# Kernel optimization log

Hardware: AMD Instinct MI355X
Metric: run time of the kernel (lower is better)

## Reference

```python
import jax, jax.numpy as jnp
import numpy as np

HIDDEN = 4096
NUM_Q = 32
NUM_KV = 8
HEAD_DIM = 128
EPS = 1e-6
ROPE_THETA = 1e6


def _rmsnorm(x, w):
    # x: [..., HEAD_DIM]
    var = jnp.mean(x * x, axis=-1, keepdims=True)
    return x * jax.lax.rsqrt(var + EPS) * w


def _rope(x, positions):
    # x: [n_tok, H, HEAD_DIM], rotate-half convention
    half = HEAD_DIM // 2
    inv_freq = 1.0 / (ROPE_THETA ** (jnp.arange(0, half, dtype=jnp.float32) / half))
    freqs = positions.astype(jnp.float32)[:, None] * inv_freq  # [n_tok, half]
    cos = jnp.concatenate([jnp.cos(freqs), jnp.cos(freqs)], axis=-1)[:, None, :]
    sin = jnp.concatenate([jnp.sin(freqs), jnp.sin(freqs)], axis=-1)[:, None, :]
    x1, x2 = x[..., :half], x[..., half:]
    rot = jnp.concatenate([-x2, x1], axis=-1)
    return x * cos + rot * sin


def setup_inputs() -> dict:
    key = jax.random.key(0)
    ks = jax.random.split(key, 7)
    n_tok = 2048
    s = 0.02
    return {
        "hidden": jax.random.normal(ks[0], (n_tok, HIDDEN), dtype=jnp.float32),
        "positions": jnp.arange(n_tok, dtype=jnp.int32),
        "Wq": jax.random.normal(ks[1], (HIDDEN, NUM_Q * HEAD_DIM), dtype=jnp.float32) * s,
        "Wk": jax.random.normal(ks[2], (HIDDEN, NUM_KV * HEAD_DIM), dtype=jnp.float32) * s,
        "Wv": jax.random.normal(ks[3], (HIDDEN, NUM_KV * HEAD_DIM), dtype=jnp.float32) * s,
        "Wo": jax.random.normal(ks[4], (NUM_Q * HEAD_DIM, HIDDEN), dtype=jnp.float32) * s,
        "q_norm_w": jnp.ones((HEAD_DIM,), dtype=jnp.float32),
        "k_norm_w": jnp.ones((HEAD_DIM,), dtype=jnp.float32),
    }


def reference(hidden, positions, Wq, Wk, Wv, Wo, q_norm_w, k_norm_w):
    n_tok = hidden.shape[0]
    group = NUM_Q // NUM_KV

    q = (hidden @ Wq).reshape(n_tok, NUM_Q, HEAD_DIM)
    k = (hidden @ Wk).reshape(n_tok, NUM_KV, HEAD_DIM)
    v = (hidden @ Wv).reshape(n_tok, NUM_KV, HEAD_DIM)

    q = _rmsnorm(q, q_norm_w)
    k = _rmsnorm(k, k_norm_w)
    q = _rope(q, positions)
    k = _rope(k, positions)

    # GQA: group q heads [n_tok, NUM_KV, group, HEAD_DIM]
    qg = q.reshape(n_tok, NUM_KV, group, HEAD_DIM)
    scale = 1.0 / np.sqrt(HEAD_DIM)
    scores = jnp.einsum("qhgd,khd->hgqk", qg, k) * scale  # [NUM_KV, group, n_tok, n_tok]
    causal = jnp.tril(jnp.ones((n_tok, n_tok), dtype=bool))
    scores = jnp.where(causal, scores, jnp.finfo(scores.dtype).min)
    probs = jax.nn.softmax(scores, axis=-1)
    out = jnp.einsum("hgqk,khd->qhgd", probs, v)  # [n_tok, NUM_KV, group, HEAD_DIM]
    out = out.reshape(n_tok, NUM_Q * HEAD_DIM)
    return out @ Wo
```

## Files before the change

kernel.cpp:

```cpp
#include <hip/hip_runtime.h>
#include <stdint.h>

typedef unsigned short u16;
typedef __bf16 bf16_t;
typedef bf16_t bf16x8 __attribute__((ext_vector_type(8)));
typedef float f32x4 __attribute__((ext_vector_type(4)));
typedef u16 u16x4 __attribute__((ext_vector_type(4)));
typedef u16 u16x8 __attribute__((ext_vector_type(8)));

#define HIDDEN 4096
#define NTOK 2048
#define NQ 32
#define NKV 8
#define HD 128
#define QKV_N 6144

#define AS1 __attribute__((address_space(1)))
#define AS3 __attribute__((address_space(3)))

__device__ __forceinline__ u16 f2bf(float f) {
  union { float f; uint32_t u; } v; v.f = f;
  uint32_t u = v.u;
  return (u16)((u + 0x7fffu + ((u >> 16) & 1u)) >> 16);
}

__global__ void cvt_hidden(const float* __restrict__ src, u16* __restrict__ dst, int n4) {
  int i = blockIdx.x * blockDim.x + threadIdx.x;
  if (i >= n4) return;
  float4 v = ((const float4*)src)[i];
  u16x4 o;
  o[0] = f2bf(v.x); o[1] = f2bf(v.y); o[2] = f2bf(v.z); o[3] = f2bf(v.w);
  ((u16x4*)dst)[i] = o;
}

__global__ void transpose_cvt(const float* __restrict__ src, u16* __restrict__ dst,
                              int R, int C) {
  __shared__ float tile[64][65];
  int tx = threadIdx.x & 63;
  int ty = threadIdx.x >> 6;
  int r0 = blockIdx.y * 64, c0 = blockIdx.x * 64;
  for (int i = 0; i < 16; i++) {
    int r = ty + i * 4;
    tile[r][tx] = src[(size_t)(r0 + r) * C + c0 + tx];
  }
  __syncthreads();
  for (int i = 0; i < 16; i++) {
    int c = ty + i * 4;
    dst[(size_t)(c0 + c) * R + r0 + tx] = f2bf(tile[tx][c]);
  }
}

__global__ __launch_bounds__(256, 3) void gemm_bt(const u16* __restrict__ A,
                                                  const u16* __restrict__ B,
                                                  float* __restrict__ C,
                                                  int M, int N, int K) {
  __shared__ u16 sA[128 * 64];
  __shared__ u16 sB[128 * 64];
  const int tid = threadIdx.x;
  const int wave = tid >> 6, lane = tid & 63;
  const int quad = lane >> 4, l16 = lane & 15;
  const int wy = wave >> 1, wx = wave & 1;
  const int row0 = blockIdx.y * 128, col0 = blockIdx.x * 128;
  f32x4 acc[4][4] = {};
  const int lr = lane >> 3;
  const int sc = (lane & 7) ^ lr;
  const u16* gA = A + (size_t)(row0 + wave * 32 + lr) * K + sc * 8;
  const u16* gB = B + (size_t)(col0 + wave * 32 + lr) * K + sc * 8;
  u16* lA = sA + wave * 32 * 64;
  u16* lB = sB + wave * 32 * 64;
  const int swz = l16 & 7;
  for (int k0 = 0; k0 < K; k0 += 64) {
    for (int j = 0; j < 4; j++) {
      __builtin_amdgcn_global_load_lds(
          (AS1 void*)(void*)(gA + k0 + (size_t)(j * 8) * K),
          (AS3 void*)(void*)(lA + j * 8 * 64), 16, 0, 0);
      __builtin_amdgcn_global_load_lds(
          (AS1 void*)(void*)(gB + k0 + (size_t)(j * 8) * K),
          (AS3 void*)(void*)(lB + j * 8 * 64), 16, 0, 0);
    }
    __syncthreads();
    bf16x8 af[2][4], bfr[2][4];
    for (int s = 0; s < 2; s++)
      for (int mi = 0; mi < 4; mi++) {
        const int c = ((s * 4 + quad) ^ swz) * 8;
        af[s][mi] = *(const bf16x8*)(const void*)(sA + (wy * 64 + mi * 16 + l16) * 64 + c);
        bfr[s][mi] = *(const bf16x8*)(const void*)(sB + (wx * 64 + mi * 16 + l16) * 64 + c);
      }
    for (int s = 0; s < 2; s++)
      for (int mi = 0; mi < 4; mi++)
        for (int ni = 0; ni < 4; ni++)
          acc[mi][ni] = __builtin_amdgcn_mfma_f32_16x16x32_bf16(af[s][mi], bfr[s][ni], acc[mi][ni], 0, 0, 0);
    __syncthreads();
  }
  for (int mi = 0; mi < 4; mi++)
    for (int ni = 0; ni < 4; ni++) {
      int row = row0 + wy * 64 + mi * 16 + quad * 4;
      int col = col0 + wx * 64 + ni * 16 + l16;
      float* cp = C + (size_t)row * N + col;
      for (int r = 0; r < 4; r++) cp[(size_t)r * N] = acc[mi][ni][r];
    }
}

__global__ void normrope(const float* __restrict__ qkv, const int* __restrict__ pos,
                         const float* __restrict__ qw, const float* __restrict__ kw,
                         u16* __restrict__ Qo, u16* __restrict__ Ko) {
  const int hh = blockIdx.x;
  const int t = blockIdx.y * 4 + (threadIdx.x >> 6);
  const int lane = threadIdx.x & 63;
  const bool isQ = hh < NQ;
  const int col = isQ ? hh * HD : HIDDEN + (hh - NQ) * HD;
  const float* src = qkv + (size_t)t * QKV_N + col;
  float x1 = src[lane], x2 = src[lane + 64];
  float ss = x1 * x1 + x2 * x2;
  for (int m = 1; m < 64; m <<= 1) ss += __shfl_xor(ss, m);
  float inv = rsqrtf(ss * (1.0f / 128.0f) + 1e-6f);
  const float* w = isQ ? qw : kw;
  x1 *= inv * w[lane];
  x2 *= inv * w[lane + 64];
  float p = (float)pos[t];
  float freq = expf((float)lane * -0.2158673525f);
  float a = p * freq;
  float sn = sinf(a), cs = cosf(a);
  float o1 = x1 * cs - x2 * sn;
  float o2 = x2 * cs + x1 * sn;
  const float osc = isQ ? 0.08838834764831845f : 1.0f;
  u16* dst = isQ ? (Qo + (size_t)t * (NQ * HD) + hh * HD)
                 : (Ko + (size_t)t * (NKV * HD) + (hh - NQ) * HD);
  dst[lane] = f2bf(o1 * osc);
  dst[lane + 64] = f2bf(o2 * osc);
}

__global__ void vtrans(const float* __restrict__ qkv, u16* __restrict__ vT) {
  __shared__ float s[128][65];
  int tb = blockIdx.x;
  int vh = blockIdx.y;
  int tid = threadIdx.x;
  for (int i = 0; i < 32; i++) {
    int e = i * 256 + tid;
    int tl = e >> 7;
    int d = e & 127;
    s[d][tl] = qkv[(size_t)(tb * 64 + tl) * QKV_N + 5120 + vh * 128 + d];
  }
  __syncthreads();
  for (int i = 0; i < 32; i++) {
    int e = i * 256 + tid;
    int d = e >> 6;
    int tl = e & 63;
    vT[(size_t)vh * (HD * NTOK) + (size_t)d * NTOK + tb * 64 + tl] = f2bf(s[d][tl]);
  }
}

__global__ __launch_bounds__(512) void flash2(const u16* __restrict__ Q,
                                              const u16* __restrict__ K,
                                              const u16* __restrict__ V,
                                              u16* __restrict__ O) {
  __shared__ u16 sK[64 * 136];
  __shared__ u16 sV[128 * 72];
  __shared__ u16 sP[8][16 * 72];
  const int p = blockIdx.x, h = blockIdx.y, kvh = h >> 2;
  const int tid = threadIdx.x;
  const int wave = tid >> 6, lane = tid & 63;
  const int quad = lane >> 4, l16 = lane & 15;
  u16* myP = &sP[wave][0];
  const u16* Vh = V + (size_t)kvh * (HD * NTOK);
  const int qtiles[2] = {p, 15 - p};
  const int rk0 = tid >> 4, ck0 = tid & 15;
  const int rv0 = tid >> 3, cv0 = tid & 7;
  for (int ti = 0; ti < 2; ti++) {
    const int qb = qtiles[ti];
    const int qrow0 = qb * 128 + wave * 16;
    bf16x8 qf[4];
    for (int ks = 0; ks < 4; ks++)
      qf[ks] = *(const bf16x8*)(const void*)(Q + (size_t)(qrow0 + l16) * (NQ * HD) + h * HD + ks * 32 + quad * 8);
    f32x4 accO[8] = {};
    float l_r[4] = {0.f, 0.f, 0.f, 0.f};
    const int nU = 2 * (qb + 1);
    const int myMax = (qrow0 + 15) >> 6;
    for (int kb = 0; kb < nU; kb++) {
      u16x8 k0 = *(const u16x8*)(const void*)(K + (size_t)(kb * 64 + rk0) * (NKV * HD) + kvh * HD + ck0 * 8);
      u16x8 k1 = *(const u16x8*)(const void*)(K + (size_t)(kb * 64 + rk0 + 32) * (NKV * HD) + kvh * HD + ck0 * 8);
      u16x8 v0 = *(const u16x8*)(const void*)(Vh + (size_t)rv0 * NTOK + kb * 64 + cv0 * 8);
      u16x8 v1 = *(const u16x8*)(const void*)(Vh + (size_t)(rv0 + 64) * NTOK + kb * 64 + cv0 * 8);
      __syncthreads();
      *(u16x8*)(void*)(sK + rk0 * 136 + ck0 * 8) = k0;
      *(u16x8*)(void*)(sK + (rk0 + 32) * 136 + ck0 * 8) = k1;
      *(u16x8*)(void*)(sV + rv0 * 72 + cv0 * 8) = v0;
      *(u16x8*)(void*)(sV + (rv0 + 64) * 72 + cv0 * 8) = v1;
      __syncthreads();
      if (kb <= myMax) {
        f32x4 s[4] = {};
        for (int ks = 0; ks < 4; ks++)
          for (int nt = 0; nt < 4; nt++) {
            bf16x8 kf = *(const bf16x8*)(const void*)(sK + (nt * 16 + l16) * 136 + ks * 32 + quad * 8);
            s[nt] = __builtin_amdgcn_mfma_f32_16x16x32_bf16(qf[ks], kf, s[nt], 0, 0, 0);
          }
        const int qg = qrow0 + quad * 4;
        for (int nt = 0; nt < 4; nt++) {
          int tok = kb * 64 + nt * 16 + l16;
          for (int r = 0; r < 4; r++) {
            float e = __expf(s[nt][r]);
            float pv = (tok <= qg + r) ? e : 0.0f;
            l_r[r] += pv;
            myP[(quad * 4 + r) * 72 + nt * 16 + l16] = f2bf(pv);
          }
        }
        asm volatile("s_waitcnt lgkmcnt(0)" ::: "memory");
        for (int ks = 0; ks < 2; ks++) {
          bf16x8 pf = *(const bf16x8*)(const void*)(myP + l16 * 72 + ks * 32 + quad * 8);
          for (int nt = 0; nt < 8; nt++) {
            bf16x8 vf = *(const bf16x8*)(const void*)(sV + (nt * 16 + l16) * 72 + ks * 32 + quad * 8);
            accO[nt] = __builtin_amdgcn_mfma_f32_16x16x32_bf16(pf, vf, accO[nt], 0, 0, 0);
          }
        }
      }
    }
    float inv[4];
    for (int r = 0; r < 4; r++) {
      float t = l_r[r];
      t += __shfl_xor(t, 1);
      t += __shfl_xor(t, 2);
      t += __shfl_xor(t, 4);
      t += __shfl_xor(t, 8);
      inv[r] = 1.0f / t;
    }
    for (int nt = 0; nt < 8; nt++)
      for (int r = 0; r < 4; r++)
        O[(size_t)(qrow0 + quad * 4 + r) * (NQ * HD) + h * HD + nt * 16 + l16] =
            f2bf(accO[nt][r] * inv[r]);
  }
}

extern "C" void kernel_launch(void* const* d_in, const int* in_sizes, int n_in,
                              void* d_out, int out_size, void* d_ws, size_t ws_size,
                              hipStream_t stream) {
  const float* hidden = (const float*)d_in[0];
  const int* positions = (const int*)d_in[1];
  const float* Wq = (const float*)d_in[2];
  const float* Wk = (const float*)d_in[3];
  const float* Wv = (const float*)d_in[4];
  const float* Wo = (const float*)d_in[5];
  const float* qw = (const float*)d_in[6];
  const float* kw = (const float*)d_in[7];
  char* ws = (char*)d_ws;
  u16* hid_bf  = (u16*)(ws);
  u16* WqkvT   = (u16*)(ws + 16777216);
  u16* WoT     = (u16*)(ws + 67108864);
  float* qkvf  = (float*)(ws + 100663296);
  u16* Qn      = (u16*)(ws + 150994944);
  u16* Kn      = (u16*)(ws + 167772160);
  u16* Vt      = (u16*)(ws + 171966464);
  u16* AO      = (u16*)(ws + 176160768);
  float* outp  = (float*)d_out;

  cvt_hidden<<<NTOK * HIDDEN / 4 / 256, 256, 0, stream>>>(hidden, hid_bf, NTOK * HIDDEN / 4);
  transpose_cvt<<<dim3(64, 64), 256, 0, stream>>>(Wq, WqkvT, 4096, 4096);
  transpose_cvt<<<dim3(16, 64), 256, 0, stream>>>(Wk, WqkvT + (size_t)4096 * 4096, 4096, 1024);
  transpose_cvt<<<dim3(16, 64), 256, 0, stream>>>(Wv, WqkvT + (size_t)5120 * 4096, 4096, 1024);
  transpose_cvt<<<dim3(64, 64), 256, 0, stream>>>(Wo, WoT, 4096, 4096);
  gemm_bt<<<dim3(48, 16), 256, 0, stream>>>(hid_bf, WqkvT, qkvf, 2048, 6144, 4096);
  normrope<<<dim3(40, 512), 256, 0, stream>>>(qkvf, positions, qw, kw, Qn, Kn);
  vtrans<<<dim3(32, 8), 256, 0, stream>>>(qkvf, Vt);
  flash2<<<dim3(8, 32), 512, 0, stream>>>(Qn, Kn, Vt, AO);
  gemm_bt<<<dim3(32, 16), 256, 0, stream>>>(AO, WoT, outp, 2048, 4096, 4096);
}
```

Baseline: 510.0 us.

## Rewrite flash attention with 32x32 MFMA, register-resident P and K/V prefetch

Replaces the flash2 attention kernel with flash3. Each wave now handles 32 query rows using 32x32x16 bf16 MFMAs, and the two balanced causal tiles are processed concurrently by wave halves instead of sequentially. The P matrix stays in registers, built with packed bf16 converts and a lane permute, instead of passing through shared memory. K/V loads for the next block are prefetched into registers during compute. Block ids are remapped so blocks sharing a KV head are adjacent. All of this aims to cut LDS traffic and serialization, at the cost of higher register pressure.

```diff
diff --git a/kernel.cpp b/kernel.cpp
--- a/kernel.cpp
+++ b/kernel.cpp
@@ -5,8 +5,11 @@
 typedef __bf16 bf16_t;
 typedef bf16_t bf16x8 __attribute__((ext_vector_type(8)));
 typedef float f32x4 __attribute__((ext_vector_type(4)));
+typedef float f32x16 __attribute__((ext_vector_type(16)));
 typedef u16 u16x4 __attribute__((ext_vector_type(4)));
 typedef u16 u16x8 __attribute__((ext_vector_type(8)));
+typedef uint32_t u32x4 __attribute__((ext_vector_type(4)));
+typedef int i32x2 __attribute__((ext_vector_type(2)));
 
 #define HIDDEN 4096
 #define NTOK 2048
@@ -150,84 +153,137 @@
   }
 }
 
-__global__ __launch_bounds__(512) void flash2(const u16* __restrict__ Q,
-                                              const u16* __restrict__ K,
-                                              const u16* __restrict__ V,
-                                              u16* __restrict__ O) {
+__global__ __launch_bounds__(512, 2) void flash3(const u16* __restrict__ Q,
+                                                 const u16* __restrict__ K,
+                                                 const u16* __restrict__ V,
+                                                 u16* __restrict__ O) {
   __shared__ u16 sK[64 * 136];
   __shared__ u16 sV[128 * 72];
-  __shared__ u16 sP[8][16 * 72];
-  const int p = blockIdx.x, h = blockIdx.y, kvh = h >> 2;
+  const int lid = blockIdx.x;
+  const int kvh = lid & 7;
+  const int head = kvh * 4 + ((lid >> 3) & 3);
+  const int p = lid >> 5;
   const int tid = threadIdx.x;
   const int wave = tid >> 6, lane = tid & 63;
-  const int quad = lane >> 4, l16 = lane & 15;
-  u16* myP = &sP[wave][0];
+  const int l32 = lane & 31, h = lane >> 5;
+  const int tileq = (wave < 4) ? p : (15 - p);
+  const int qrow0 = tileq * 128 + (wave & 3) * 32;
   const u16* Vh = V + (size_t)kvh * (HD * NTOK);
-  const int qtiles[2] = {p, 15 - p};
+
+  bf16x8 qf[8];
+  const u16* qbase = Q + (size_t)(qrow0 + l32) * (NQ * HD) + head * HD + h * 8;
+#pragma unroll
+  for (int ks = 0; ks < 8; ks++)
+    qf[ks] = *(const bf16x8*)(const void*)(qbase + ks * 16);
+
+  f32x16 accO[4] = {};
+  float l_loc = 0.f;
+  const int nU = 32 - 2 * p;
   const int rk0 = tid >> 4, ck0 = tid & 15;
   const int rv0 = tid >> 3, cv0 = tid & 7;
-  for (int ti = 0; ti < 2; ti++) {
-    const int qb = qtiles[ti];
-    const int qrow0 = qb * 128 + wave * 16;
-    bf16x8 qf[4];
-    for (int ks = 0; ks < 4; ks++)
-      qf[ks] = *(const bf16x8*)(const void*)(Q + (size_t)(qrow0 + l16) * (NQ * HD) + h * HD + ks * 32 + quad * 8);
-    f32x4 accO[8] = {};
-    float l_r[4] = {0.f, 0.f, 0.f, 0.f};
-    const int nU = 2 * (qb + 1);
-    const int myMax = (qrow0 + 15) >> 6;
-    for (int kb = 0; kb < nU; kb++) {
-      u16x8 k0 = *(const u16x8*)(const void*)(K + (size_t)(kb * 64 + rk0) * (NKV * HD) + kvh * HD + ck0 * 8);
-      u16x8 k1 = *(const u16x8*)(const void*)(K + (size_t)(kb * 64 + rk0 + 32) * (NKV * HD) + kvh * HD + ck0 * 8);
-      u16x8 v0 = *(const u16x8*)(const void*)(Vh + (size_t)rv0 * NTOK + kb * 64 + cv0 * 8);
-      u16x8 v1 = *(const u16x8*)(const void*)(Vh + (size_t)(rv0 + 64) * NTOK + kb * 64 + cv0 * 8);
-      __syncthreads();
-      *(u16x8*)(void*)(sK + rk0 * 136 + ck0 * 8) = k0;
-      *(u16x8*)(void*)(sK + (rk0 + 32) * 136 + ck0 * 8) = k1;
-      *(u16x8*)(void*)(sV + rv0 * 72 + cv0 * 8) = v0;
-      *(u16x8*)(void*)(sV + (rv0 + 64) * 72 + cv0 * 8) = v1;
-      __syncthreads();
-      if (kb <= myMax) {
-        f32x4 s[4] = {};
-        for (int ks = 0; ks < 4; ks++)
-          for (int nt = 0; nt < 4; nt++) {
-            bf16x8 kf = *(const bf16x8*)(const void*)(sK + (nt * 16 + l16) * 136 + ks * 32 + quad * 8);
-            s[nt] = __builtin_amdgcn_mfma_f32_16x16x32_bf16(qf[ks], kf, s[nt], 0, 0, 0);
-          }
-        const int qg = qrow0 + quad * 4;
-        for (int nt = 0; nt < 4; nt++) {
-          int tok = kb * 64 + nt * 16 + l16;
-          for (int r = 0; r < 4; r++) {
-            float e = __expf(s[nt][r]);
-            float pv = (tok <= qg + r) ? e : 0.0f;
-            l_r[r] += pv;
-            myP[(quad * 4 + r) * 72 + nt * 16 + l16] = f2bf(pv);
-          }
-        }
-        asm volatile("s_waitcnt lgkmcnt(0)" ::: "memory");
-        for (int ks = 0; ks < 2; ks++) {
-          bf16x8 pf = *(const bf16x8*)(const void*)(myP + l16 * 72 + ks * 32 + quad * 8);
-          for (int nt = 0; nt < 8; nt++) {
-            bf16x8 vf = *(const bf16x8*)(const void*)(sV + (nt * 16 + l16) * 72 + ks * 32 + quad * 8);
-            accO[nt] = __builtin_amdgcn_mfma_f32_16x16x32_bf16(pf, vf, accO[nt], 0, 0, 0);
-          }
+  const u16* Kr = K + (size_t)kvh * HD + ck0 * 8;
+  const u16* Vr = Vh + (size_t)rv0 * NTOK + cv0 * 8;
+  const u16* Vr2 = Vh + (size_t)(rv0 + 64) * NTOK + cv0 * 8;
+
+  u16x8 k0 = *(const u16x8*)(const void*)(Kr + (size_t)rk0 * (NKV * HD));
+  u16x8 k1 = *(const u16x8*)(const void*)(Kr + (size_t)(rk0 + 32) * (NKV * HD));
+  u16x8 v0 = *(const u16x8*)(const void*)(Vr);
+  u16x8 v1 = *(const u16x8*)(const void*)(Vr2);
+
+  for (int kb = 0; kb < nU; kb++) {
+    __syncthreads();
+    *(u16x8*)(void*)(sK + rk0 * 136 + ck0 * 8) = k0;
+    *(u16x8*)(void*)(sK + (rk0 + 32) * 136 + ck0 * 8) = k1;
+    *(u16x8*)(void*)(sV + rv0 * 72 + cv0 * 8) = v0;
+    *(u16x8*)(void*)(sV + (rv0 + 64) * 72 + cv0 * 8) = v1;
+    __syncthreads();
+    if (kb + 1 < nU) {
+      const size_t koff = (size_t)((kb + 1) * 64) * (NKV * HD);
+      k0 = *(const u16x8*)(const void*)(Kr + koff + (size_t)rk0 * (NKV * HD));
+      k1 = *(const u16x8*)(const void*)(Kr + koff + (size_t)(rk0 + 32) * (NKV * HD));
+      v0 = *(const u16x8*)(const void*)(Vr + (kb + 1) * 64);
+      v1 = *(const u16x8*)(const void*)(Vr2 + (kb + 1) * 64);
+    }
+    const int t0 = kb * 64;
+    if (t0 > qrow0 + 31) continue;
+    const bool act1 = (t0 + 32 <= qrow0 + 31);
+
+    f32x16 s0 = {}, s1 = {};
+#pragma unroll
+    for (int ks = 0; ks < 8; ks++) {
+      bf16x8 kf0 = *(const bf16x8*)(const void*)(sK + l32 * 136 + ks * 16 + h * 8);
+      s0 = __builtin_amdgcn_mfma_f32_32x32x16_bf16(kf0, qf[ks], s0, 0, 0, 0);
+    }
+    if (act1) {
+#pragma unroll
+      for (int ks = 0; ks < 8; ks++) {
+        bf16x8 kf1 = *(const bf16x8*)(const void*)(sK + (32 + l32) * 136 + ks * 16 + h * 8);
+        s1 = __builtin_amdgcn_mfma_f32_32x32x16_bf16(kf1, qf[ks], s1, 0, 0, 0);
+      }
+    }
+
+    auto process = [&](const f32x16& sv_, int tb) {
+      float pr[16];
+      const int tbase = t0 + tb * 32;
+      const int qg = qrow0 + l32;
+      if (tbase + 31 <= qrow0) {
+#pragma unroll
+        for (int r = 0; r < 16; r++) { float e = __expf(sv_[r]); pr[r] = e; l_loc += e; }
+      } else {
+#pragma unroll
+        for (int r = 0; r < 16; r++) {
+          const int tok = tbase + (r & 3) + 8 * (r >> 2) + 4 * h;
+          float e = (tok <= qg) ? __expf(sv_[r]) : 0.f;
+          pr[r] = e; l_loc += e;
         }
       }
-    }
-    float inv[4];
-    for (int r = 0; r < 4; r++) {
-      float t = l_r[r];
-      t += __shfl_xor(t, 1);
-      t += __shfl_xor(t, 2);
-      t += __shfl_xor(t, 4);
-      t += __shfl_xor(t, 8);
-      inv[r] = 1.0f / t;
-    }
-    for (int nt = 0; nt < 8; nt++)
-      for (int r = 0; r < 4; r++)
-        O[(size_t)(qrow0 + quad * 4 + r) * (NQ * HD) + h * HD + nt * 16 + l16] =
-            f2bf(accO[nt][r] * inv[r]);
-  }
+#pragma unroll
+      for (int u = 0; u < 2; u++) {
+        uint32_t A0, A1, B0, B1;
+        asm("v_cvt_pk_bf16_f32 %0, %1, %2" : "=v"(A0) : "v"(pr[u * 8 + 0]), "v"(pr[u * 8 + 1]));
+        asm("v_cvt_pk_bf16_f32 %0, %1, %2" : "=v"(A1) : "v"(pr[u * 8 + 2]), "v"(pr[u * 8 + 3]));
+        asm("v_cvt_pk_bf16_f32 %0, %1, %2" : "=v"(B0) : "v"(pr[u * 8 + 4]), "v"(pr[u * 8 + 5]));
+        asm("v_cvt_pk_bf16_f32 %0, %1, %2" : "=v"(B1) : "v"(pr[u * 8 + 6]), "v"(pr[u * 8 + 7]));
+#if __has_builtin(__builtin_amdgcn_permlane32_swap)
+        i32x2 r02 = __builtin_amdgcn_permlane32_swap((int)A0, (int)B0, false, false);
+        i32x2 r13 = __builtin_amdgcn_permlane32_swap((int)A1, (int)B1, false, false);
+        const uint32_t w0 = (uint32_t)r02.x, w2 = (uint32_t)r02.y;
+        const uint32_t w1 = (uint32_t)r13.x, w3 = (uint32_t)r13.y;
+#else
+        const uint32_t A0x = (uint32_t)__shfl_xor((int)A0, 32);
+        const uint32_t A1x = (uint32_t)__shfl_xor((int)A1, 32);
+        const uint32_t B0x = (uint32_t)__shfl_xor((int)B0, 32);
+        const uint32_t B1x = (uint32_t)__shfl_xor((int)B1, 32);
+        const uint32_t w0 = h ? B0x : A0;
+        const uint32_t w1 = h ? B1x : A1;
+        const uint32_t w2 = h ? B0 : A0x;
+        const uint32_t w3 = h ? B1 : A1x;
+#endif
+        union { u32x4 w; bf16x8 v; } pf;
+        pf.w = (u32x4){w0, w1, w2, w3};
+#pragma unroll
+        for (int db = 0; db < 4; db++) {
+          bf16x8 vf = *(const bf16x8*)(const void*)(sV + (db * 32 + l32) * 72 + tb * 32 + u * 16 + h * 8);
+          accO[db] = __builtin_amdgcn_mfma_f32_32x32x16_bf16(vf, pf.v, accO[db], 0, 0, 0);
+        }
+      }
+    };
+    process(s0, 0);
+    if (act1) process(s1, 1);
+  }
+
+  l_loc += __shfl_xor(l_loc, 32);
+  const float inv = 1.0f / l_loc;
+  u16* ob = O + (size_t)(qrow0 + l32) * (NQ * HD) + head * HD;
+#pragma unroll
+  for (int db = 0; db < 4; db++)
+#pragma unroll
+    for (int g = 0; g < 4; g++) {
+      u16x4 o4;
+#pragma unroll
+      for (int j = 0; j < 4; j++) o4[j] = f2bf(accO[db][4 * g + j] * inv);
+      *(u16x4*)(void*)(ob + db * 32 + g * 8 + h * 4) = o4;
+    }
 }
 
 extern "C" void kernel_launch(void* const* d_in, const int* in_sizes, int n_in,
@@ -260,6 +316,6 @@
   gemm_bt<<<dim3(48, 16), 256, 0, stream>>>(hid_bf, WqkvT, qkvf, 2048, 6144, 4096);
   normrope<<<dim3(40, 512), 256, 0, stream>>>(qkvf, positions, qw, kw, Qn, Kn);
   vtrans<<<dim3(32, 8), 256, 0, stream>>>(qkvf, Vt);
-  flash2<<<dim3(8, 32), 512, 0, stream>>>(Qn, Kn, Vt, AO);
+  flash3<<<dim3(256), 512, 0, stream>>>(Qn, Kn, Vt, AO);
   gemm_bt<<<dim3(32, 16), 256, 0, stream>>>(AO, WoT, outp, 2048, 4096, 4096);
 }
```

Measured after the change: 479.3 us. -6.0%, faster.
